# Kernel optimization log

Measured on AMD Instinct MI355X. Metric: run time of the kernel, lower is better.

Reference implementation:

```python
import jax, jax.numpy as jnp
import numpy as np

NB, NLOC, DIN, DOUT = 4, 4096, 512, 512
NTYPES, TEBD = 128, 128
N_EXPERTS, TOP_K = 8, 2  # share_expert = 0 -> routed_experts = 8, routed_top_k = 2


def setup_inputs() -> dict:
    key = jax.random.key(0)
    k = jax.random.split(key, 6)
    return {
        "x": jax.random.normal(k[0], (NB, NLOC, DIN), dtype=jnp.float32),
        "type_embeddings": jax.random.normal(k[1], (NTYPES, TEBD), dtype=jnp.float32),
        "atom_types": jax.random.randint(k[2], (NB, NLOC), 0, NTYPES, dtype=jnp.int32),
        "Wg": jax.random.normal(k[3], (TEBD, N_EXPERTS), dtype=jnp.float32) / np.sqrt(TEBD),
        "We": jax.random.normal(k[4], (N_EXPERTS, DIN, DOUT), dtype=jnp.float32) / np.sqrt(DIN),
        "be": jax.random.normal(k[5], (N_EXPERTS, DOUT), dtype=jnp.float32) * 0.01,
    }


def reference(x, type_embeddings, atom_types, Wg, We, be):
    # --- route: gate on type embeddings, then index per atom (MD-continuous) ---
    logits = type_embeddings @ Wg                       # [ntypes, E]
    top_vals, top_idx = jax.lax.top_k(logits, TOP_K)    # [ntypes, K]
    weights = jax.nn.softmax(top_vals, axis=-1)         # softmax over selected logits
    atom_w = weights[atom_types]                        # [nb, nloc, K]
    atom_i = top_idx[atom_types]                        # [nb, nloc, K]

    # scatter-add top-k weights into dense per-expert weights (matches scatter_add_)
    onehot = jax.nn.one_hot(atom_i, N_EXPERTS, dtype=x.dtype)   # [nb, nloc, K, E]
    per_expert_w = jnp.einsum("bnk,bnke->bne", atom_w, onehot)  # [nb, nloc, E]

    # --- run all experts densely (the batched JIT-friendly path), then combine ---
    expert_out = jnp.tanh(jnp.einsum("bnd,edo->bneo", x, We) + be)  # [nb, nloc, E, dout]
    out = jnp.einsum("bne,bneo->bno", per_expert_w, expert_out)     # [nb, nloc, dout]
    return out
```

## Files before the change

### kernel.cpp

```cpp
#include <hip/hip_runtime.h>
#include <hip/hip_bf16.h>
#include <math.h>

typedef __bf16 bf16;
typedef __bf16 bf16x8 __attribute__((ext_vector_type(8)));
typedef float  f32x4  __attribute__((ext_vector_type(4)));

#define NTOK   16384
#define DIN    512
#define DOUT   512
#define NTYPES 128
#define TEBD   128
#define NEXP   8
#define NPAIR  64
#define MAXTILE 192

#define WS_HPART   0
#define WS_ROUTE_W 32768
#define WS_BASET   33792
#define WS_CURS    34304
#define WS_CNTP    34816
#define WS_BASEP   35072
#define WS_NTILE   35328
#define WS_TMAP    35840
#define WS_RMAP    37888
#define WS_WGT     (WS_RMAP + NTOK * 4)
#define WS_XG      (WS_WGT + NTOK * 8)
#define WS_WET     (WS_XG + (size_t)NTOK * DIN * 2)

#define GLOAD_LDS16(g, l)                                                     \
  __builtin_amdgcn_global_load_lds(                                           \
      (const __attribute__((address_space(1))) void*)(g),                     \
      (__attribute__((address_space(3))) void*)(l), 16, 0, 0)

__global__ void hist_kernel(const int* __restrict__ atype, int* __restrict__ hpart) {
  __shared__ int h[NTYPES];
  int tid = threadIdx.x;
  if (tid < NTYPES) h[tid] = 0;
  __syncthreads();
  int t = blockIdx.x * 256 + tid;
  atomicAdd(&h[atype[t]], 1);
  __syncthreads();
  if (tid < NTYPES) hpart[tid * 64 + blockIdx.x] = h[tid];
}

__global__ void route_scan_kernel(const float* __restrict__ emb,
                                  const float* __restrict__ Wg,
                                  const int* __restrict__ hpart,
                                  float* __restrict__ route_w,
                                  int* __restrict__ base_type,
                                  int* __restrict__ cursor,
                                  int* __restrict__ cnt_pair,
                                  int* __restrict__ base_pair,
                                  int* __restrict__ ntile,
                                  int* __restrict__ tmap) {
  __shared__ int s_cnt[NPAIR];
  __shared__ int s_off[NTYPES];
  __shared__ int s_pair[NTYPES];
  int t = threadIdx.x;
  if (t < NPAIR) s_cnt[t] = 0;
  __syncthreads();

  int myc = 0;
  {
    const int4* hp = (const int4*)(hpart + t * 64);
#pragma unroll
    for (int b = 0; b < 16; ++b) {
      int4 v = hp[b];
      myc += v.x + v.y + v.z + v.w;
    }
  }

  const float* er = emb + (size_t)t * TEBD;
  float lg[NEXP];
#pragma unroll
  for (int e = 0; e < NEXP; ++e) lg[e] = 0.f;
  for (int j = 0; j < TEBD; ++j) {
    float ev = er[j];
#pragma unroll
    for (int e = 0; e < NEXP; ++e) lg[e] += ev * Wg[j * NEXP + e];
  }
  float v0 = -__builtin_inff(), v1 = -__builtin_inff();
  int i0 = 0, i1 = 0;
#pragma unroll
  for (int e = 0; e < NEXP; ++e) {
    float v = lg[e];
    if (v > v0) { v1 = v0; i1 = i0; v0 = v; i0 = e; }
    else if (v > v1) { v1 = v; i1 = e; }
  }
  float d = expf(v1 - v0);
  float inv = 1.f / (1.f + d);
  route_w[t * 2 + 0] = inv;
  route_w[t * 2 + 1] = d * inv;
  int p = i0 * 8 + i1;
  s_pair[t] = p;
  s_off[t] = atomicAdd(&s_cnt[p], myc);
  cursor[t] = 0;
  __syncthreads();

  if (t < NPAIR) {
    int b = 0, tb = 0;
    for (int j = 0; j < t; ++j) { b += s_cnt[j]; tb += (s_cnt[j] + 127) >> 7; }
    base_pair[t] = b;
    cnt_pair[t] = s_cnt[t];
    int nt_l = (s_cnt[t] + 127) >> 7;
    for (int i = 0; i < nt_l; ++i) {
      tmap[(tb + i) * 2 + 0] = t;
      tmap[(tb + i) * 2 + 1] = i * 128;
    }
    if (t == NPAIR - 1) ntile[0] = tb + nt_l;
  }
  __syncthreads();
  base_type[t] = base_pair[s_pair[t]] + s_off[t];
}

__global__ void prep_kernel(const float* __restrict__ x,
                            const float* __restrict__ We,
                            const int* __restrict__ atype,
                            const float* __restrict__ route_w,
                            const int* __restrict__ base_type,
                            int* __restrict__ cursor,
                            int* __restrict__ row_map,
                            float* __restrict__ wgt,
                            bf16* __restrict__ xg,
                            bf16* __restrict__ WeT) {
  int bx = blockIdx.x;
  int tid = threadIdx.x;
  if (bx < 256) {
    __shared__ int posS[64];
    int t0 = bx * 64;
    if (tid < 64) {
      int t = t0 + tid;
      int ty = atype[t];
      int pos = base_type[ty] + atomicAdd(&cursor[ty], 1);
      posS[tid] = pos;
      row_map[pos] = t;
      ((float2*)wgt)[pos] = ((const float2*)route_w)[ty];
    }
    __syncthreads();
    int w = tid >> 6, lane = tid & 63;
#pragma unroll
    for (int i = 0; i < 16; ++i) {
      int r = w * 16 + i;
      const float4* p = (const float4*)(x + (size_t)(t0 + r) * DIN + lane * 8);
      float4 a = p[0], b = p[1];
      bf16x8 o;
      o[0] = (bf16)a.x; o[1] = (bf16)a.y; o[2] = (bf16)a.z; o[3] = (bf16)a.w;
      o[4] = (bf16)b.x; o[5] = (bf16)b.y; o[6] = (bf16)b.z; o[7] = (bf16)b.w;
      *(bf16x8*)(xg + (size_t)posS[r] * DIN + lane * 8) = o;
    }
  } else {
    __shared__ float t[64][65];
    int b2 = bx - 256;
    int e = b2 >> 6;
    int rem = b2 & 63;
    int kt = (rem >> 3) * 64;
    int nt = (rem & 7) * 64;
    int col = tid & 63;
    int rq = tid >> 6;
#pragma unroll
    for (int r = 0; r < 16; ++r) {
      int row = rq * 16 + r;
      t[row][col] = We[((size_t)e * DIN + kt + row) * DOUT + nt + col];
    }
    __syncthreads();
#pragma unroll
    for (int r = 0; r < 16; ++r) {
      int n = rq * 16 + r;
      WeT[((size_t)e * DOUT + nt + n) * DIN + kt + col] = (bf16)t[col][n];
    }
  }
}

__global__ __launch_bounds__(256, 2) void moe_gemm_pair_kernel(
    const bf16* __restrict__ xg, const bf16* __restrict__ WeT,
    const float* __restrict__ be, const int* __restrict__ cnt_pair,
    const int* __restrict__ base_pair, const int* __restrict__ ntile,
    const int* __restrict__ tmap, const int* __restrict__ row_map,
    const float* __restrict__ wgt, float* __restrict__ out) {
  int nwork = ntile[0] * 8;
  int f = blockIdx.y * 8 + blockIdx.x;
  if (f >= nwork) return;
  int q = nwork >> 3, r = nwork & 7;
  int xcd = f & 7, idx = f >> 3;
  int L = (xcd < r ? xcd * (q + 1) : r * (q + 1) + (xcd - r) * q) + idx;
  int ti = L >> 3;
  int cx = L & 7;
  int list = tmap[ti * 2 + 0];
  int r0   = tmap[ti * 2 + 1];
  int e0 = list >> 3, e1 = list & 7;
  int nrow = cnt_pair[list] - r0;
  if (nrow > 128) nrow = 128;
  int c0 = cx * 64;
  int arow0 = base_pair[list] + r0;

  __shared__ __align__(16) bf16 As[4][128 * 32];
  __shared__ __align__(16) bf16 B0s[4][64 * 32];
  __shared__ __align__(16) bf16 B1s[4][64 * 32];
  __shared__ int   tokS[128];
  __shared__ float w0S[128], w1S[128];
  __shared__ float be0S[64], be1S[64];

  int tid = threadIdx.x;
  int lane = tid & 63, w = tid >> 6;

  const bf16* srcA[2];
#pragma unroll
  for (int j = 0; j < 2; ++j) {
    int slot = w * 128 + j * 64 + lane;
    int row = slot >> 2, cs = slot & 3;
    int c = cs ^ ((row >> 1) & 3);
    int srow = (row < nrow) ? row : (nrow - 1);
    srcA[j] = xg + (size_t)(arow0 + srow) * DIN + c * 8;
  }
  const bf16* srcB0;
  const bf16* srcB1;
  {
    int slot = w * 64 + lane;
    int row = slot >> 2, cs = slot & 3;
    int c = cs ^ ((row >> 1) & 3);
    srcB0 = WeT + ((size_t)e0 * DOUT + c0 + row) * DIN + c * 8;
    srcB1 = WeT + ((size_t)e1 * DOUT + c0 + row) * DIN + c * 8;
  }

  auto stage = [&](int buf) {
#pragma unroll
    for (int j = 0; j < 2; ++j) {
      GLOAD_LDS16(srcA[j], &As[buf][(w * 128 + j * 64) * 8]);
      srcA[j] += 32;
    }
    GLOAD_LDS16(srcB0, &B0s[buf][w * 64 * 8]);
    GLOAD_LDS16(srcB1, &B1s[buf][w * 64 * 8]);
    srcB0 += 32;
    srcB1 += 32;
  };

  stage(0);
  stage(1);
  stage(2);

  if (tid < 128) {
    int srow = (tid < nrow) ? tid : (nrow - 1);
    int gl = arow0 + srow;
    tokS[tid] = row_map[gl];
    float2 ww = ((const float2*)wgt)[gl];
    w0S[tid] = ww.x;
    w1S[tid] = ww.y;
    if (tid < 64) {
      be0S[tid] = be[e0 * DOUT + c0 + tid];
      be1S[tid] = be[e1 * DOUT + c0 + tid];
    }
  }

  f32x4 acc0[4][2], acc1[4][2];
#pragma unroll
  for (int mi = 0; mi < 4; ++mi)
#pragma unroll
    for (int ni = 0; ni < 2; ++ni) { acc0[mi][ni] = (f32x4)0.f; acc1[mi][ni] = (f32x4)0.f; }

  int wm = (w >> 1) * 64;
  int wn = (w & 1) * 32;
  int r16 = lane & 15, g16 = lane >> 4;

  int offA[4], offB[2];
#pragma unroll
  for (int i = 0; i < 4; ++i) {
    int rA = wm + i * 16 + r16;
    offA[i] = rA * 32 + (g16 ^ ((rA >> 1) & 3)) * 8;
  }
#pragma unroll
  for (int i = 0; i < 2; ++i) {
    int rB = wn + i * 16 + r16;
    offB[i] = rB * 32 + (g16 ^ ((rB >> 1) & 3)) * 8;
  }

#pragma unroll
  for (int t = 0; t < 16; ++t) {
    if (t < 14)      asm volatile("s_waitcnt vmcnt(8)" ::: "memory");
    else if (t == 14) asm volatile("s_waitcnt vmcnt(4)" ::: "memory");
    else              asm volatile("s_waitcnt vmcnt(0)" ::: "memory");
    __builtin_amdgcn_s_barrier();
    if (t + 3 < 16) stage((t + 3) & 3);

    int cur = t & 3;
    bf16x8 af[4], b0f[2], b1f[2];
#pragma unroll
    for (int i = 0; i < 4; ++i) af[i] = *(const bf16x8*)&As[cur][offA[i]];
#pragma unroll
    for (int i = 0; i < 2; ++i) b0f[i] = *(const bf16x8*)&B0s[cur][offB[i]];
#pragma unroll
    for (int i = 0; i < 2; ++i) b1f[i] = *(const bf16x8*)&B1s[cur][offB[i]];
    __builtin_amdgcn_s_setprio(1);
#pragma unroll
    for (int mi = 0; mi < 4; ++mi)
#pragma unroll
      for (int ni = 0; ni < 2; ++ni) {
        acc0[mi][ni] = __builtin_amdgcn_mfma_f32_16x16x32_bf16(
            af[mi], b0f[ni], acc0[mi][ni], 0, 0, 0);
        acc1[mi][ni] = __builtin_amdgcn_mfma_f32_16x16x32_bf16(
            af[mi], b1f[ni], acc1[mi][ni], 0, 0, 0);
      }
    __builtin_amdgcn_s_setprio(0);
  }

#pragma unroll
  for (int mi = 0; mi < 4; ++mi) {
#pragma unroll
    for (int ni = 0; ni < 2; ++ni) {
      f32x4 v0 = acc0[mi][ni];
      f32x4 v1 = acc1[mi][ni];
      int colLocal = wn + ni * 16 + r16;
      float bev0 = be0S[colLocal];
      float bev1 = be1S[colLocal];
#pragma unroll
      for (int r = 0; r < 4; ++r) {
        int lrow = wm + mi * 16 + g16 * 4 + r;
        if (lrow < nrow) {
          float x0 = fminf(9.f, fmaxf(-9.f, v0[r] + bev0)) * 2.885390082f;
          float x1 = fminf(9.f, fmaxf(-9.f, v1[r] + bev1)) * 2.885390082f;
          float e0v, e1v, invd;
          asm("v_exp_f32 %0, %1" : "=v"(e0v) : "v"(x0));
          asm("v_exp_f32 %0, %1" : "=v"(e1v) : "v"(x1));
          float d0 = e0v + 1.f, d1 = e1v + 1.f;
          asm("v_rcp_f32 %0, %1" : "=v"(invd) : "v"(d0 * d1));
          float t0 = (e0v - 1.f) * d1 * invd;
          float t1 = (e1v - 1.f) * d0 * invd;
          out[(size_t)tokS[lrow] * DOUT + c0 + colLocal] =
              t0 * w0S[lrow] + t1 * w1S[lrow];
        }
      }
    }
  }
}

extern "C" void kernel_launch(void* const* d_in, const int* in_sizes, int n_in,
                              void* d_out, int out_size, void* d_ws, size_t ws_size,
                              hipStream_t stream) {
  const float* x    = (const float*)d_in[0];
  const float* emb  = (const float*)d_in[1];
  const int*   aty  = (const int*)d_in[2];
  const float* Wg   = (const float*)d_in[3];
  const float* We   = (const float*)d_in[4];
  const float* be   = (const float*)d_in[5];
  float* out = (float*)d_out;

  char* ws = (char*)d_ws;
  int*   hpart     = (int*)(ws + WS_HPART);
  float* route_w   = (float*)(ws + WS_ROUTE_W);
  int*   base_type = (int*)(ws + WS_BASET);
  int*   cursor    = (int*)(ws + WS_CURS);
  int*   cnt_pair  = (int*)(ws + WS_CNTP);
  int*   base_pair = (int*)(ws + WS_BASEP);
  int*   ntile     = (int*)(ws + WS_NTILE);
  int*   tmap      = (int*)(ws + WS_TMAP);
  int*   row_map   = (int*)(ws + WS_RMAP);
  float* wgt       = (float*)(ws + WS_WGT);
  bf16*  xg        = (bf16*)(ws + WS_XG);
  bf16*  WeT       = (bf16*)(ws + WS_WET);

  hist_kernel<<<NTOK / 256, 256, 0, stream>>>(aty, hpart);
  route_scan_kernel<<<1, 128, 0, stream>>>(emb, Wg, hpart, route_w, base_type,
                                           cursor, cnt_pair, base_pair, ntile, tmap);
  prep_kernel<<<256 + 512, 256, 0, stream>>>(x, We, aty, route_w, base_type,
                                             cursor, row_map, wgt, xg, WeT);
  moe_gemm_pair_kernel<<<dim3(8, MAXTILE), 256, 0, stream>>>(
      xg, WeT, be, cnt_pair, base_pair, ntile, tmap, row_map, wgt, out);
}
```

Before: 82.95 us.

## Load GEMM operands directly from global into registers, dropping LDS staging

```diff
diff --git a/kernel.cpp b/kernel.cpp
--- a/kernel.cpp
+++ b/kernel.cpp
@@ -27,11 +27,6 @@
 #define WS_WGT     (WS_RMAP + NTOK * 4)
 #define WS_XG      (WS_WGT + NTOK * 8)
 #define WS_WET     (WS_XG + (size_t)NTOK * DIN * 2)
-
-#define GLOAD_LDS16(g, l)                                                     \
-  __builtin_amdgcn_global_load_lds(                                           \
-      (const __attribute__((address_space(1))) void*)(g),                     \
-      (__attribute__((address_space(3))) void*)(l), 16, 0, 0)
 
 __global__ void hist_kernel(const int* __restrict__ atype, int* __restrict__ hpart) {
   __shared__ int h[NTYPES];
@@ -172,7 +167,7 @@
   }
 }
 
-__global__ __launch_bounds__(256, 2) void moe_gemm_pair_kernel(
+__global__ __launch_bounds__(256, 3) void moe_gemm_pair_kernel(
     const bf16* __restrict__ xg, const bf16* __restrict__ WeT,
     const float* __restrict__ be, const int* __restrict__ cnt_pair,
     const int* __restrict__ base_pair, const int* __restrict__ ntile,
@@ -194,50 +189,12 @@
   int c0 = cx * 64;
   int arow0 = base_pair[list] + r0;
 
-  __shared__ __align__(16) bf16 As[4][128 * 32];
-  __shared__ __align__(16) bf16 B0s[4][64 * 32];
-  __shared__ __align__(16) bf16 B1s[4][64 * 32];
   __shared__ int   tokS[128];
   __shared__ float w0S[128], w1S[128];
   __shared__ float be0S[64], be1S[64];
 
   int tid = threadIdx.x;
   int lane = tid & 63, w = tid >> 6;
-
-  const bf16* srcA[2];
-#pragma unroll
-  for (int j = 0; j < 2; ++j) {
-    int slot = w * 128 + j * 64 + lane;
-    int row = slot >> 2, cs = slot & 3;
-    int c = cs ^ ((row >> 1) & 3);
-    int srow = (row < nrow) ? row : (nrow - 1);
-    srcA[j] = xg + (size_t)(arow0 + srow) * DIN + c * 8;
-  }
-  const bf16* srcB0;
-  const bf16* srcB1;
-  {
-    int slot = w * 64 + lane;
-    int row = slot >> 2, cs = slot & 3;
-    int c = cs ^ ((row >> 1) & 3);
-    srcB0 = WeT + ((size_t)e0 * DOUT + c0 + row) * DIN + c * 8;
-    srcB1 = WeT + ((size_t)e1 * DOUT + c0 + row) * DIN + c * 8;
-  }
-
-  auto stage = [&](int buf) {
-#pragma unroll
-    for (int j = 0; j < 2; ++j) {
-      GLOAD_LDS16(srcA[j], &As[buf][(w * 128 + j * 64) * 8]);
-      srcA[j] += 32;
-    }
-    GLOAD_LDS16(srcB0, &B0s[buf][w * 64 * 8]);
-    GLOAD_LDS16(srcB1, &B1s[buf][w * 64 * 8]);
-    srcB0 += 32;
-    srcB1 += 32;
-  };
-
-  stage(0);
-  stage(1);
-  stage(2);
 
   if (tid < 128) {
     int srow = (tid < nrow) ? tid : (nrow - 1);
@@ -252,56 +209,69 @@
     }
   }
 
-  f32x4 acc0[4][2], acc1[4][2];
-#pragma unroll
-  for (int mi = 0; mi < 4; ++mi)
-#pragma unroll
-    for (int ni = 0; ni < 2; ++ni) { acc0[mi][ni] = (f32x4)0.f; acc1[mi][ni] = (f32x4)0.f; }
-
   int wm = (w >> 1) * 64;
   int wn = (w & 1) * 32;
   int r16 = lane & 15, g16 = lane >> 4;
 
-  int offA[4], offB[2];
+  const bf16* pA[4];
 #pragma unroll
   for (int i = 0; i < 4; ++i) {
-    int rA = wm + i * 16 + r16;
-    offA[i] = rA * 32 + (g16 ^ ((rA >> 1) & 3)) * 8;
-  }
+    int rowA = wm + i * 16 + r16;
+    int srow = (rowA < nrow) ? rowA : (nrow - 1);
+    pA[i] = xg + (size_t)(arow0 + srow) * DIN + g16 * 8;
+  }
+  const bf16* pB0[2];
+  const bf16* pB1[2];
 #pragma unroll
   for (int i = 0; i < 2; ++i) {
-    int rB = wn + i * 16 + r16;
-    offB[i] = rB * 32 + (g16 ^ ((rB >> 1) & 3)) * 8;
-  }
-
-#pragma unroll
-  for (int t = 0; t < 16; ++t) {
-    if (t < 14)      asm volatile("s_waitcnt vmcnt(8)" ::: "memory");
-    else if (t == 14) asm volatile("s_waitcnt vmcnt(4)" ::: "memory");
-    else              asm volatile("s_waitcnt vmcnt(0)" ::: "memory");
-    __builtin_amdgcn_s_barrier();
-    if (t + 3 < 16) stage((t + 3) & 3);
-
-    int cur = t & 3;
-    bf16x8 af[4], b0f[2], b1f[2];
-#pragma unroll
-    for (int i = 0; i < 4; ++i) af[i] = *(const bf16x8*)&As[cur][offA[i]];
-#pragma unroll
-    for (int i = 0; i < 2; ++i) b0f[i] = *(const bf16x8*)&B0s[cur][offB[i]];
-#pragma unroll
-    for (int i = 0; i < 2; ++i) b1f[i] = *(const bf16x8*)&B1s[cur][offB[i]];
-    __builtin_amdgcn_s_setprio(1);
-#pragma unroll
-    for (int mi = 0; mi < 4; ++mi)
-#pragma unroll
-      for (int ni = 0; ni < 2; ++ni) {
-        acc0[mi][ni] = __builtin_amdgcn_mfma_f32_16x16x32_bf16(
-            af[mi], b0f[ni], acc0[mi][ni], 0, 0, 0);
-        acc1[mi][ni] = __builtin_amdgcn_mfma_f32_16x16x32_bf16(
-            af[mi], b1f[ni], acc1[mi][ni], 0, 0, 0);
-      }
-    __builtin_amdgcn_s_setprio(0);
-  }
+    int colB = wn + i * 16 + r16;
+    pB0[i] = WeT + ((size_t)e0 * DOUT + c0 + colB) * DIN + g16 * 8;
+    pB1[i] = WeT + ((size_t)e1 * DOUT + c0 + colB) * DIN + g16 * 8;
+  }
+
+  f32x4 acc0[4][2], acc1[4][2];
+#pragma unroll
+  for (int mi = 0; mi < 4; ++mi)
+#pragma unroll
+    for (int ni = 0; ni < 2; ++ni) { acc0[mi][ni] = (f32x4)0.f; acc1[mi][ni] = (f32x4)0.f; }
+
+  bf16x8 aX[4], b0X[2], b1X[2];
+  bf16x8 aY[4], b0Y[2], b1Y[2];
+
+#define LOADSET(A, B0, B1, kk)                                                \
+  {                                                                           \
+    _Pragma("unroll") for (int i = 0; i < 4; ++i)                             \
+        A[i] = *(const bf16x8*)(pA[i] + (kk) * 32);                           \
+    _Pragma("unroll") for (int i = 0; i < 2; ++i)                             \
+        B0[i] = *(const bf16x8*)(pB0[i] + (kk) * 32);                         \
+    _Pragma("unroll") for (int i = 0; i < 2; ++i)                             \
+        B1[i] = *(const bf16x8*)(pB1[i] + (kk) * 32);                         \
+  }
+
+#define MFMASET(A, B0, B1)                                                    \
+  {                                                                           \
+    _Pragma("unroll") for (int mi = 0; mi < 4; ++mi)                          \
+        _Pragma("unroll") for (int ni = 0; ni < 2; ++ni) {                    \
+      acc0[mi][ni] = __builtin_amdgcn_mfma_f32_16x16x32_bf16(                 \
+          A[mi], B0[ni], acc0[mi][ni], 0, 0, 0);                              \
+      acc1[mi][ni] = __builtin_amdgcn_mfma_f32_16x16x32_bf16(                 \
+          A[mi], B1[ni], acc1[mi][ni], 0, 0, 0);                              \
+    }                                                                         \
+  }
+
+  LOADSET(aX, b0X, b1X, 0);
+  LOADSET(aY, b0Y, b1Y, 1);
+#pragma unroll
+  for (int t = 0; t < 16; t += 2) {
+    MFMASET(aX, b0X, b1X);
+    if (t + 2 < 16) LOADSET(aX, b0X, b1X, t + 2);
+    MFMASET(aY, b0Y, b1Y);
+    if (t + 3 < 16) LOADSET(aY, b0Y, b1Y, t + 3);
+  }
+#undef LOADSET
+#undef MFMASET
+
+  __syncthreads();
 
 #pragma unroll
   for (int mi = 0; mi < 4; ++mi) {
```

After: 157.6 us. 89.9% more time.

## Convert x to bf16 in natural order and gather rows in GEMM via row map

Applied to the files above, without the earlier changes.

```diff
diff --git a/kernel.cpp b/kernel.cpp
--- a/kernel.cpp
+++ b/kernel.cpp
@@ -24,24 +24,63 @@
 #define WS_NTILE   35328
 #define WS_TMAP    35840
 #define WS_RMAP    37888
-#define WS_WGT     (WS_RMAP + NTOK * 4)
-#define WS_XG      (WS_WGT + NTOK * 8)
-#define WS_WET     (WS_XG + (size_t)NTOK * DIN * 2)
+#define WS_WGT     (WS_RMAP + MAXTILE * 128 * 4)
+#define WS_XB      (WS_WGT + MAXTILE * 128 * 8)
+#define WS_WET     (WS_XB + (size_t)NTOK * DIN * 2)
 
 #define GLOAD_LDS16(g, l)                                                     \
   __builtin_amdgcn_global_load_lds(                                           \
       (const __attribute__((address_space(1))) void*)(g),                     \
       (__attribute__((address_space(3))) void*)(l), 16, 0, 0)
 
-__global__ void hist_kernel(const int* __restrict__ atype, int* __restrict__ hpart) {
-  __shared__ int h[NTYPES];
+__global__ void fused_prep_kernel(const float* __restrict__ x,
+                                  const float* __restrict__ We,
+                                  const int* __restrict__ atype,
+                                  int* __restrict__ hpart,
+                                  bf16* __restrict__ xb,
+                                  bf16* __restrict__ WeT) {
+  int bx = blockIdx.x;
   int tid = threadIdx.x;
-  if (tid < NTYPES) h[tid] = 0;
-  __syncthreads();
-  int t = blockIdx.x * 256 + tid;
-  atomicAdd(&h[atype[t]], 1);
-  __syncthreads();
-  if (tid < NTYPES) hpart[tid * 64 + blockIdx.x] = h[tid];
+  if (bx < 64) {
+    __shared__ int h[NTYPES];
+    if (tid < NTYPES) h[tid] = 0;
+    __syncthreads();
+    int t = bx * 256 + tid;
+    atomicAdd(&h[atype[t]], 1);
+    __syncthreads();
+    if (tid < NTYPES) hpart[tid * 64 + bx] = h[tid];
+  } else if (bx < 576) {
+    __shared__ float t[64][65];
+    int b2 = bx - 64;
+    int e = b2 >> 6;
+    int rem = b2 & 63;
+    int kt = (rem >> 3) * 64;
+    int nt = (rem & 7) * 64;
+    int col = tid & 63;
+    int rq = tid >> 6;
+#pragma unroll
+    for (int r = 0; r < 16; ++r) {
+      int row = rq * 16 + r;
+      t[row][col] = We[((size_t)e * DIN + kt + row) * DOUT + nt + col];
+    }
+    __syncthreads();
+#pragma unroll
+    for (int r = 0; r < 16; ++r) {
+      int n = rq * 16 + r;
+      WeT[((size_t)e * DOUT + nt + n) * DIN + kt + col] = (bf16)t[col][n];
+    }
+  } else {
+    size_t base = (size_t)(bx - 576) * 4096 + tid * 16;
+    const float4* p = (const float4*)(x + base);
+    float4 a0 = p[0], a1 = p[1], a2 = p[2], a3 = p[3];
+    bf16x8 o0, o1;
+    o0[0] = (bf16)a0.x; o0[1] = (bf16)a0.y; o0[2] = (bf16)a0.z; o0[3] = (bf16)a0.w;
+    o0[4] = (bf16)a1.x; o0[5] = (bf16)a1.y; o0[6] = (bf16)a1.z; o0[7] = (bf16)a1.w;
+    o1[0] = (bf16)a2.x; o1[1] = (bf16)a2.y; o1[2] = (bf16)a2.z; o1[3] = (bf16)a2.w;
+    o1[4] = (bf16)a3.x; o1[5] = (bf16)a3.y; o1[6] = (bf16)a3.z; o1[7] = (bf16)a3.w;
+    *(bf16x8*)(xb + base) = o0;
+    *(bf16x8*)(xb + base + 8) = o1;
+  }
 }
 
 __global__ void route_scan_kernel(const float* __restrict__ emb,
@@ -53,7 +92,8 @@
                                   int* __restrict__ cnt_pair,
                                   int* __restrict__ base_pair,
                                   int* __restrict__ ntile,
-                                  int* __restrict__ tmap) {
+                                  int* __restrict__ tmap,
+                                  int* __restrict__ row_map) {
   __shared__ int s_cnt[NPAIR];
   __shared__ int s_off[NTYPES];
   __shared__ int s_pair[NTYPES];
@@ -100,7 +140,11 @@
 
   if (t < NPAIR) {
     int b = 0, tb = 0;
-    for (int j = 0; j < t; ++j) { b += s_cnt[j]; tb += (s_cnt[j] + 127) >> 7; }
+    for (int j = 0; j < t; ++j) {
+      int nt_j = (s_cnt[j] + 127) >> 7;
+      b += nt_j << 7;
+      tb += nt_j;
+    }
     base_pair[t] = b;
     cnt_pair[t] = s_cnt[t];
     int nt_l = (s_cnt[t] + 127) >> 7;
@@ -108,76 +152,41 @@
       tmap[(tb + i) * 2 + 0] = t;
       tmap[(tb + i) * 2 + 1] = i * 128;
     }
+    for (int i = s_cnt[t]; i < (nt_l << 7); ++i) row_map[b + i] = 0;
     if (t == NPAIR - 1) ntile[0] = tb + nt_l;
   }
   __syncthreads();
   base_type[t] = base_pair[s_pair[t]] + s_off[t];
 }
 
-__global__ void prep_kernel(const float* __restrict__ x,
-                            const float* __restrict__ We,
-                            const int* __restrict__ atype,
-                            const float* __restrict__ route_w,
-                            const int* __restrict__ base_type,
-                            int* __restrict__ cursor,
-                            int* __restrict__ row_map,
-                            float* __restrict__ wgt,
-                            bf16* __restrict__ xg,
-                            bf16* __restrict__ WeT) {
-  int bx = blockIdx.x;
+__global__ void place_kernel(const int* __restrict__ atype,
+                             const float* __restrict__ route_w,
+                             const int* __restrict__ base_type,
+                             int* __restrict__ cursor,
+                             int* __restrict__ row_map,
+                             float* __restrict__ wgt) {
+  __shared__ int lc[NTYPES];
+  __shared__ int lb[NTYPES];
   int tid = threadIdx.x;
-  if (bx < 256) {
-    __shared__ int posS[64];
-    int t0 = bx * 64;
-    if (tid < 64) {
-      int t = t0 + tid;
-      int ty = atype[t];
-      int pos = base_type[ty] + atomicAdd(&cursor[ty], 1);
-      posS[tid] = pos;
-      row_map[pos] = t;
-      ((float2*)wgt)[pos] = ((const float2*)route_w)[ty];
-    }
-    __syncthreads();
-    int w = tid >> 6, lane = tid & 63;
-#pragma unroll
-    for (int i = 0; i < 16; ++i) {
-      int r = w * 16 + i;
-      const float4* p = (const float4*)(x + (size_t)(t0 + r) * DIN + lane * 8);
-      float4 a = p[0], b = p[1];
-      bf16x8 o;
-      o[0] = (bf16)a.x; o[1] = (bf16)a.y; o[2] = (bf16)a.z; o[3] = (bf16)a.w;
-      o[4] = (bf16)b.x; o[5] = (bf16)b.y; o[6] = (bf16)b.z; o[7] = (bf16)b.w;
-      *(bf16x8*)(xg + (size_t)posS[r] * DIN + lane * 8) = o;
-    }
-  } else {
-    __shared__ float t[64][65];
-    int b2 = bx - 256;
-    int e = b2 >> 6;
-    int rem = b2 & 63;
-    int kt = (rem >> 3) * 64;
-    int nt = (rem & 7) * 64;
-    int col = tid & 63;
-    int rq = tid >> 6;
-#pragma unroll
-    for (int r = 0; r < 16; ++r) {
-      int row = rq * 16 + r;
-      t[row][col] = We[((size_t)e * DIN + kt + row) * DOUT + nt + col];
-    }
-    __syncthreads();
-#pragma unroll
-    for (int r = 0; r < 16; ++r) {
-      int n = rq * 16 + r;
-      WeT[((size_t)e * DOUT + nt + n) * DIN + kt + col] = (bf16)t[col][n];
-    }
-  }
+  if (tid < NTYPES) lc[tid] = 0;
+  __syncthreads();
+  int t = blockIdx.x * 256 + tid;
+  int ty = atype[t];
+  int r = atomicAdd(&lc[ty], 1);
+  __syncthreads();
+  if (tid < NTYPES) lb[tid] = lc[tid] ? atomicAdd(&cursor[tid], lc[tid]) : 0;
+  __syncthreads();
+  int pos = base_type[ty] + lb[ty] + r;
+  row_map[pos] = t;
+  ((float2*)wgt)[pos] = ((const float2*)route_w)[ty];
 }
 
 __global__ __launch_bounds__(256, 2) void moe_gemm_pair_kernel(
-    const bf16* __restrict__ xg, const bf16* __restrict__ WeT,
+    const bf16* __restrict__ xb, const bf16* __restrict__ WeT,
     const float* __restrict__ be, const int* __restrict__ cnt_pair,
-    const int* __restrict__ base_pair, const int* __restrict__ ntile,
-    const int* __restrict__ tmap, const int* __restrict__ row_map,
-    const float* __restrict__ wgt, float* __restrict__ out) {
+    const int* __restrict__ ntile, const int* __restrict__ tmap,
+    const int* __restrict__ row_map, const float* __restrict__ wgt,
+    float* __restrict__ out) {
   int nwork = ntile[0] * 8;
   int f = blockIdx.y * 8 + blockIdx.x;
   if (f >= nwork) return;
@@ -192,7 +201,7 @@
   int nrow = cnt_pair[list] - r0;
   if (nrow > 128) nrow = 128;
   int c0 = cx * 64;
-  int arow0 = base_pair[list] + r0;
+  int arow0 = ti * 128;
 
   __shared__ __align__(16) bf16 As[4][128 * 32];
   __shared__ __align__(16) bf16 B0s[4][64 * 32];
@@ -204,14 +213,26 @@
   int tid = threadIdx.x;
   int lane = tid & 63, w = tid >> 6;
 
+  if (tid < 128) {
+    int srow = (tid < nrow) ? tid : (nrow - 1);
+    tokS[tid] = row_map[arow0 + srow];
+    float2 ww = ((const float2*)wgt)[arow0 + srow];
+    w0S[tid] = ww.x;
+    w1S[tid] = ww.y;
+    if (tid < 64) {
+      be0S[tid] = be[e0 * DOUT + c0 + tid];
+      be1S[tid] = be[e1 * DOUT + c0 + tid];
+    }
+  }
+  __syncthreads();
+
   const bf16* srcA[2];
 #pragma unroll
   for (int j = 0; j < 2; ++j) {
     int slot = w * 128 + j * 64 + lane;
     int row = slot >> 2, cs = slot & 3;
     int c = cs ^ ((row >> 1) & 3);
-    int srow = (row < nrow) ? row : (nrow - 1);
-    srcA[j] = xg + (size_t)(arow0 + srow) * DIN + c * 8;
+    srcA[j] = xb + (size_t)tokS[row] * DIN + c * 8;
   }
   const bf16* srcB0;
   const bf16* srcB1;
@@ -238,19 +259,6 @@
   stage(0);
   stage(1);
   stage(2);
-
-  if (tid < 128) {
-    int srow = (tid < nrow) ? tid : (nrow - 1);
-    int gl = arow0 + srow;
-    tokS[tid] = row_map[gl];
-    float2 ww = ((const float2*)wgt)[gl];
-    w0S[tid] = ww.x;
-    w1S[tid] = ww.y;
-    if (tid < 64) {
-      be0S[tid] = be[e0 * DOUT + c0 + tid];
-      be1S[tid] = be[e1 * DOUT + c0 + tid];
-    }
-  }
 
   f32x4 acc0[4][2], acc1[4][2];
 #pragma unroll
@@ -355,14 +363,15 @@
   int*   tmap      = (int*)(ws + WS_TMAP);
   int*   row_map   = (int*)(ws + WS_RMAP);
   float* wgt       = (float*)(ws + WS_WGT);
-  bf16*  xg        = (bf16*)(ws + WS_XG);
+  bf16*  xb        = (bf16*)(ws + WS_XB);
   bf16*  WeT       = (bf16*)(ws + WS_WET);
 
-  hist_kernel<<<NTOK / 256, 256, 0, stream>>>(aty, hpart);
+  fused_prep_kernel<<<2624, 256, 0, stream>>>(x, We, aty, hpart, xb, WeT);
   route_scan_kernel<<<1, 128, 0, stream>>>(emb, Wg, hpart, route_w, base_type,
-                                           cursor, cnt_pair, base_pair, ntile, tmap);
-  prep_kernel<<<256 + 512, 256, 0, stream>>>(x, We, aty, route_w, base_type,
-                                             cursor, row_map, wgt, xg, WeT);
+                                           cursor, cnt_pair, base_pair, ntile,
+                                           tmap, row_map);
+  place_kernel<<<NTOK / 256, 256, 0, stream>>>(aty, route_w, base_type, cursor,
+                                               row_map, wgt);
   moe_gemm_pair_kernel<<<dim3(8, MAXTILE), 256, 0, stream>>>(
-      xg, WeT, be, cnt_pair, base_pair, ntile, tmap, row_map, wgt, out);
-}
+      xb, WeT, be, cnt_pair, ntile, tmap, row_map, wgt, out);
+}
```

After: 74.83 us. 1.11x faster.
